# Kernel optimization log

Measured on AMD Instinct MI355X. Metric: run time of the kernel, lower is better.

The kernel has to match this reference:

```python
import jax, jax.numpy as jnp
import numpy as np

B, S, D = 32, 1, 2048
H, KVH, HD = 16, 4, 128
MAXS = 4096
EPS = 1e-5
NREP = H // KVH  # GQA repeat factor = 4
FF = 4 * D
POS = 4095  # decode position (start_pos)


def setup_inputs() -> dict:
    key = jax.random.key(0)
    ks = jax.random.split(key, 12)
    sc = lambda d: 1.0 / np.sqrt(d)
    # RoPE angles for the current token position, [S, HD//2]
    inv_freq = 1.0 / (10000.0 ** (np.arange(0, HD, 2, dtype=np.float32) / HD))
    ang = (POS + np.arange(S, dtype=np.float32))[:, None] * inv_freq[None, :]
    return {
        "x": jax.random.normal(ks[0], (B, S, D), jnp.float32),
        "cos": jnp.asarray(np.cos(ang), jnp.float32),
        "sin": jnp.asarray(np.sin(ang), jnp.float32),
        "k_cache": jax.random.normal(ks[1], (B, MAXS, KVH, HD), jnp.float32),
        "v_cache": jax.random.normal(ks[2], (B, MAXS, KVH, HD), jnp.float32),
        "w_rms_attn": jnp.ones((D,), jnp.float32),
        "wq": jax.random.normal(ks[3], (D, D), jnp.float32) * sc(D),
        "wk": jax.random.normal(ks[4], (D, KVH * HD), jnp.float32) * sc(D),
        "wv": jax.random.normal(ks[5], (D, KVH * HD), jnp.float32) * sc(D),
        "wo": jax.random.normal(ks[6], (D, D), jnp.float32) * sc(D),
        "w_rms_ffn": jnp.ones((D,), jnp.float32),
        "w1": jax.random.normal(ks[7], (D, FF), jnp.float32) * sc(D),
        "w2": jax.random.normal(ks[8], (D, FF), jnp.float32) * sc(D),
        "w3": jax.random.normal(ks[9], (FF, D), jnp.float32) * sc(FF),
        "start_pos": POS,
    }


def _rmsnorm(x, g):
    return x * g * jax.lax.rsqrt(jnp.mean(x * x, axis=-1, keepdims=True) + EPS)


def _rope(x, cos, sin):
    # x: [B, S, h, HD]; complex rotation on (even, odd) pairs
    xr = x.reshape(*x.shape[:-1], HD // 2, 2)
    x0, x1 = xr[..., 0], xr[..., 1]
    c = cos[None, :, None, :]
    s = sin[None, :, None, :]
    r0 = x0 * c - x1 * s
    r1 = x0 * s + x1 * c
    return jnp.stack([r0, r1], axis=-1).reshape(x.shape)


def reference(x, cos, sin, k_cache, v_cache, w_rms_attn, wq, wk, wv, wo,
              w_rms_ffn, w1, w2, w3, start_pos):
    xa = _rmsnorm(x, w_rms_attn)
    xq = (xa @ wq).reshape(B, S, H, HD)
    xk = (xa @ wk).reshape(B, S, KVH, HD)
    xv = (xa @ wv).reshape(B, S, KVH, HD)
    # Source applies RoPE to K and V (not Q) -- reproduced faithfully.
    xk = _rope(xk, cos, sin)
    xv = _rope(xv, cos, sin)
    kc = jax.lax.dynamic_update_slice(k_cache, xk, (0, start_pos, 0, 0))
    vc = jax.lax.dynamic_update_slice(v_cache, xv, (0, start_pos, 0, 0))
    klen = start_pos + S
    keys = jnp.repeat(kc[:, :klen], NREP, axis=2)   # [B, klen, H, HD]
    vals = jnp.repeat(vc[:, :klen], NREP, axis=2)
    att = jnp.einsum('bqhd,bkhd->bhqk', xq, keys) * (HD ** -0.5)
    att = jax.nn.softmax(att, axis=-1)
    y = jnp.einsum('bhqk,bkhd->bqhd', att, vals).reshape(B, S, D)
    h = x + y @ wo
    xf = _rmsnorm(h, w_rms_ffn)
    return h + (jax.nn.silu(xf @ w1) * (xf @ w2)) @ w3
```

## Files before the change

kernel.cpp:

```cpp
#include <hip/hip_runtime.h>
#include <math.h>

#define BB 32
#define DD 2048
#define NKVH 4
#define HDIM 128
#define MAXS 4096
#define FFD 8192
#define POS 4095
#define EPSV 1e-5f
#define SCALE 0.08838834764831845f
#define ASPLIT 32
#define SPOS 128

#define OFF_QT   0u
#define OFF_KT   65536u
#define OFF_VT   81920u
#define OFF_G1   98304u
#define OFF_G2   360448u
#define ZERO_N   622592u
#define OFF_XAT  622592u
#define OFF_PML  720896u
#define OFF_PACC 753664u
#define OFF_YT   2850816u
#define OFF_H    2916352u
#define OFF_XFT  2981888u
#define OFF_KFIX 3047424u
#define OFF_VFIX 3309568u

#define VM_WAIT8  asm volatile("s_waitcnt vmcnt(8)" ::: "memory")
#define VM_WAIT0  asm volatile("s_waitcnt vmcnt(0)" ::: "memory")
#define LG_WAIT0  asm volatile("s_waitcnt lgkmcnt(0)" ::: "memory")
#define SCHED0    __builtin_amdgcn_sched_barrier(0)
#define SBAR      __builtin_amdgcn_s_barrier()

#define REP32(M) M(0) M(1) M(2) M(3) M(4) M(5) M(6) M(7) M(8) M(9) M(10) M(11) M(12) M(13) M(14) M(15) M(16) M(17) M(18) M(19) M(20) M(21) M(22) M(23) M(24) M(25) M(26) M(27) M(28) M(29) M(30) M(31)
#define REP32A(M,X) M(0,X) M(1,X) M(2,X) M(3,X) M(4,X) M(5,X) M(6,X) M(7,X) M(8,X) M(9,X) M(10,X) M(11,X) M(12,X) M(13,X) M(14,X) M(15,X) M(16,X) M(17,X) M(18,X) M(19,X) M(20,X) M(21,X) M(22,X) M(23,X) M(24,X) M(25,X) M(26,X) M(27,X) M(28,X) M(29,X) M(30,X) M(31,X)

#define DECLA(i) float a##i = 0.f;
#define FMA1(i,k) a##i = fmaf(ap[(k)*32 + (i)], w##k, a##i);
#define STORET(i) tl[i] = a##i;
#define ATOMN(i) atomicAdd(C + (size_t)(i)*N + n, a##i);

template<int N, int CH, bool TOUT>
__device__ __forceinline__ void gemv_body(const float* __restrict__ At,
                                          const float* __restrict__ W,
                                          float* __restrict__ C, int colblk,
                                          float* tile) {
    int tid = (int)threadIdx.x;
    int n = colblk * 256 + tid;
    int d0 = blockIdx.y * CH;
    const float* Wp = W + (size_t)d0 * N + n;
    const float* ap = At + (size_t)d0 * 32;
    REP32(DECLA)
#pragma unroll 4
    for (int dd = 0; dd < CH; dd += 4) {
        float w0 = Wp[0];
        float w1 = Wp[(size_t)N];
        float w2 = Wp[(size_t)N * 2];
        float w3 = Wp[(size_t)N * 3];
        REP32A(FMA1, 0)
        REP32A(FMA1, 1)
        REP32A(FMA1, 2)
        REP32A(FMA1, 3)
        Wp += (size_t)N * 4;
        ap += 128;
    }
    if constexpr (TOUT) {
        float* tl = tile + tid * 33;
        REP32(STORET)
        __syncthreads();
        float* cb = C + (size_t)colblk * 256 * 32;
#pragma unroll
        for (int i = 0; i < 32; ++i) {
            int f = i * 256 + tid;
            atomicAdd(cb + f, tile[(f >> 5) * 33 + (f & 31)]);
        }
    } else {
        REP32(ATOMN)
    }
}

template<int N, int CH, bool TOUT>
__global__ __launch_bounds__(256) void gemv32_kernel(const float* __restrict__ At,
                                                     const float* __restrict__ W,
                                                     float* __restrict__ C) {
    if constexpr (TOUT) {
        __shared__ float tile[256 * 33];
        gemv_body<N, CH, true>(At, W, C, blockIdx.x, tile);
    } else {
        gemv_body<N, CH, false>(At, W, C, blockIdx.x, nullptr);
    }
}

template<int N, int CH, int HALF>
__global__ __launch_bounds__(256) void gemv32_dual_kernel(const float* __restrict__ At,
        const float* __restrict__ W0, const float* __restrict__ W1,
        float* __restrict__ C0, float* __restrict__ C1) {
    __shared__ float tile[256 * 33];
    int bx = blockIdx.x;
    if (bx < HALF) gemv_body<N, CH, true>(At, W0, C0, bx, tile);
    else           gemv_body<N, CH, true>(At, W1, C1, bx - HALF, tile);
}

__global__ void zero_rms_kernel(float* __restrict__ p, const float* __restrict__ in,
                                const float* __restrict__ g, float* __restrict__ outT,
                                float* __restrict__ cpy) {
    int bx = blockIdx.x, tid = threadIdx.x;
    if (bx < 608) {
        ((float4*)p)[bx * 256 + tid] = (float4){0.f, 0.f, 0.f, 0.f};
        return;
    }
    int b = bx - 608;
    const float* row = in + b * DD;
    float v[8];
    float ss = 0.f;
#pragma unroll
    for (int i = 0; i < 8; ++i) { v[i] = row[tid + i * 256]; ss += v[i] * v[i]; }
#pragma unroll
    for (int off = 32; off; off >>= 1) ss += __shfl_xor(ss, off);
    __shared__ float red[4];
    if ((tid & 63) == 0) red[tid >> 6] = ss;
    __syncthreads();
    ss = red[0] + red[1] + red[2] + red[3];
    float scale = rsqrtf(ss * (1.f / DD) + EPSV);
#pragma unroll
    for (int i = 0; i < 8; ++i) {
        int idx = tid + i * 256;
        outT[(size_t)idx * 32 + b] = v[i] * g[idx] * scale;
        cpy[b * DD + idx] = v[i];
    }
}

__global__ void rmsnorm_kernel(const float* __restrict__ in, const float* __restrict__ g,
                               float* __restrict__ outT, float* __restrict__ cpy) {
    int b = blockIdx.x;
    int tid = threadIdx.x;
    const float* row = in + b * DD;
    float v[8];
    float ss = 0.f;
#pragma unroll
    for (int i = 0; i < 8; ++i) { v[i] = row[tid + i * 256]; ss += v[i] * v[i]; }
#pragma unroll
    for (int off = 32; off; off >>= 1) ss += __shfl_xor(ss, off);
    __shared__ float red[4];
    if ((tid & 63) == 0) red[tid >> 6] = ss;
    __syncthreads();
    ss = red[0] + red[1] + red[2] + red[3];
    float scale = rsqrtf(ss * (1.f / DD) + EPSV);
#pragma unroll
    for (int i = 0; i < 8; ++i) {
        int idx = tid + i * 256;
        outT[(size_t)idx * 32 + b] = v[i] * g[idx] * scale;
        if (cpy) cpy[b * DD + idx] = v[i];
    }
}

__global__ void fixrope_kernel(const float* __restrict__ kc, const float* __restrict__ vc,
                               const float* __restrict__ kT, const float* __restrict__ vT,
                               const float* __restrict__ cosb, const float* __restrict__ sinb,
                               float* __restrict__ kfix, float* __restrict__ vfix) {
    int idx = blockIdx.x * 256 + threadIdx.x;
    int b = idx >> 12, rem = idx & 4095;
    int pos = rem >> 8, pr = rem & 255;
    int gpos = 4080 + pos;
    float2 kv, vv;
    if (gpos == POS) {
        int hd2 = pr & 63;
        float c = cosb[hd2], s = sinb[hd2];
        int col = pr * 2;
        float k0 = kT[(size_t)col * 32 + b], k1 = kT[(size_t)(col + 1) * 32 + b];
        float v0 = vT[(size_t)col * 32 + b], v1 = vT[(size_t)(col + 1) * 32 + b];
        kv = (float2){k0 * c - k1 * s, k0 * s + k1 * c};
        vv = (float2){v0 * c - v1 * s, v0 * s + v1 * c};
    } else {
        size_t o = ((size_t)(b * MAXS + gpos)) * 256 + pr;
        kv = ((const float2*)kc)[o]; vv = ((const float2*)vc)[o];
    }
    size_t d = (size_t)b * 4096 + pos * 256 + pr;
    ((float2*)kfix)[d] = kv; ((float2*)vfix)[d] = vv;
}

__global__ __launch_bounds__(256, 2) void attn_stage_kernel(
    const float* __restrict__ qn, const float* __restrict__ kc, const float* __restrict__ vc,
    const float* __restrict__ kfix, const float* __restrict__ vfix,
    float* __restrict__ pml, float* __restrict__ pacc) {
    int split = blockIdx.x & 31, b = blockIdx.x >> 5;
    int tid = threadIdx.x, lane = tid & 63, wv = tid >> 6;
    __shared__ float kbuf[2][8192];
    __shared__ float p_s[128][16];
    int qpos = tid >> 4, qhead = tid & 15;
    int qr = qpos * 4 + (qhead >> 2);
    int vh = tid >> 4, c16 = tid & 15, vkvh = vh >> 2;
    int t0 = split * SPOS;

    float4 qrot[32];
#pragma unroll
    for (int j = 0; j < 32; ++j) {
        int g = (j + qr) & 31;
        qrot[j] = *(const float4*)(qn + (size_t)b * DD + qhead * HDIM + g * 4);
    }
    float4 av0 = {0, 0, 0, 0}, av1 = {0, 0, 0, 0};

    auto stage = [&](int t) {
        int s = t & 7;
        const float* base;
        if (t < 8) base = (split == 31 && s == 7) ? kfix + (size_t)b * 8192
                                                  : kc + ((size_t)b * MAXS + t0 + s * 16) * 512;
        else       base = (split == 31 && s == 7) ? vfix + (size_t)b * 8192
                                                  : vc + ((size_t)b * MAXS + t0 + s * 16) * 512;
        const float* g = base + wv * 2048 + lane * 4;
        float* l = &kbuf[t & 1][wv * 2048];
#pragma unroll
        for (int i = 0; i < 8; ++i)
            __builtin_amdgcn_global_load_lds(
                (const __attribute__((address_space(1))) void*)(g + i * 256),
                (__attribute__((address_space(3))) void*)(l + i * 256), 16, 0, 0);
    };

    stage(0);
    for (int t = 0; t < 16; ++t) {
        if (t < 15) { stage(t + 1); VM_WAIT8; } else { VM_WAIT0; }
        SCHED0; SBAR;
        if (t == 8) {
#pragma unroll
            for (int hh = 0; hh < 4; ++hh) {
                int h = wv * 4 + hh;
                float e0 = p_s[lane][h], e1 = p_s[lane + 64][h];
                float m = fmaxf(e0, e1);
#pragma unroll
                for (int off = 32; off; off >>= 1) m = fmaxf(m, __shfl_xor(m, off));
                e0 = __expf(e0 - m); e1 = __expf(e1 - m);
                p_s[lane][h] = e0; p_s[lane + 64][h] = e1;
                float l2 = e0 + e1;
#pragma unroll
                for (int off = 32; off; off >>= 1) l2 += __shfl_xor(l2, off);
                if (lane == 0) {
                    int idx = ((b * ASPLIT + split) * 16 + h) * 2;
                    pml[idx] = m; pml[idx + 1] = l2;
                }
            }
        }
        const float* kb = kbuf[t & 1];
        if (t < 8) {
            float4 acc = {0, 0, 0, 0};
            const float* rowp = kb + qr * 128;
#pragma unroll
            for (int j = 0; j < 32; ++j) {
                int g = (j + qr) & 31;
                float4 k4 = *(const float4*)(rowp + g * 4);
                acc.x = fmaf(k4.x, qrot[j].x, acc.x);
                acc.y = fmaf(k4.y, qrot[j].y, acc.y);
                acc.z = fmaf(k4.z, qrot[j].z, acc.z);
                acc.w = fmaf(k4.w, qrot[j].w, acc.w);
            }
            p_s[t * 16 + qpos][qhead] = (acc.x + acc.y + acc.z + acc.w) * SCALE;
        } else {
            int s = t - 8;
            const float* vrow = kb + vkvh * 128 + c16 * 4;
#pragma unroll
            for (int p = 0; p < 16; ++p) {
                float pw = p_s[s * 16 + p][vh];
                float4 v0 = *(const float4*)(vrow + p * 512);
                float4 v1 = *(const float4*)(vrow + p * 512 + 64);
                av0.x = fmaf(pw, v0.x, av0.x); av0.y = fmaf(pw, v0.y, av0.y);
                av0.z = fmaf(pw, v0.z, av0.z); av0.w = fmaf(pw, v0.w, av0.w);
                av1.x = fmaf(pw, v1.x, av1.x); av1.y = fmaf(pw, v1.y, av1.y);
                av1.z = fmaf(pw, v1.z, av1.z); av1.w = fmaf(pw, v1.w, av1.w);
            }
        }
        LG_WAIT0; SCHED0; SBAR;
    }
    size_t pbase = ((size_t)(b * ASPLIT + split) * 16 + vh) * HDIM;
    *(float4*)(pacc + pbase + c16 * 4) = av0;
    *(float4*)(pacc + pbase + 64 + c16 * 4) = av1;
}

__global__ void attn_combine_kernel(const float* __restrict__ pml,
                                    const float* __restrict__ pacc, float* __restrict__ yT) {
    int bid = blockIdx.x;
    int b = bid >> 4, h = bid & 15;
    int d = threadIdx.x;
    float M = -INFINITY;
#pragma unroll 8
    for (int s = 0; s < ASPLIT; ++s)
        M = fmaxf(M, pml[((b * ASPLIT + s) * 16 + h) * 2]);
    float denom = 0.f, acc = 0.f;
#pragma unroll 4
    for (int s = 0; s < ASPLIT; ++s) {
        int idx = (b * ASPLIT + s) * 16 + h;
        float e = __expf(pml[idx * 2] - M);
        denom += pml[idx * 2 + 1] * e;
        acc += e * pacc[(size_t)idx * HDIM + d];
    }
    yT[(size_t)(h * HDIM + d) * 32 + b] = acc / denom;
}

__global__ void silu_mul_kernel(float* __restrict__ g1, const float* __restrict__ g2) {
    int i = blockIdx.x * 256 + threadIdx.x;
    float4 a = ((const float4*)g1)[i];
    float4 b4 = ((const float4*)g2)[i];
    a.x = a.x * b4.x / (1.f + __expf(-a.x));
    a.y = a.y * b4.y / (1.f + __expf(-a.y));
    a.z = a.z * b4.z / (1.f + __expf(-a.z));
    a.w = a.w * b4.w / (1.f + __expf(-a.w));
    ((float4*)g1)[i] = a;
}

extern "C" void kernel_launch(void* const* d_in, const int* in_sizes, int n_in,
                              void* d_out, int out_size, void* d_ws, size_t ws_size,
                              hipStream_t stream) {
    (void)in_sizes; (void)n_in; (void)out_size; (void)ws_size;
    const float* x    = (const float*)d_in[0];
    const float* cosb = (const float*)d_in[1];
    const float* sinb = (const float*)d_in[2];
    const float* kc   = (const float*)d_in[3];
    const float* vc   = (const float*)d_in[4];
    const float* wra  = (const float*)d_in[5];
    const float* wq   = (const float*)d_in[6];
    const float* wk   = (const float*)d_in[7];
    const float* wv   = (const float*)d_in[8];
    const float* wo   = (const float*)d_in[9];
    const float* wrf  = (const float*)d_in[10];
    const float* w1   = (const float*)d_in[11];
    const float* w2   = (const float*)d_in[12];
    const float* w3   = (const float*)d_in[13];
    float* out = (float*)d_out;
    float* ws  = (float*)d_ws;

    float* qn   = ws + OFF_QT;
    float* kT   = ws + OFF_KT;
    float* vT   = ws + OFF_VT;
    float* g1T  = ws + OFF_G1;
    float* g2T  = ws + OFF_G2;
    float* xaT  = ws + OFF_XAT;
    float* pml  = ws + OFF_PML;
    float* pacc = ws + OFF_PACC;
    float* yT   = ws + OFF_YT;
    float* h    = ws + OFF_H;
    float* xfT  = ws + OFF_XFT;
    float* kfix = ws + OFF_KFIX;
    float* vfix = ws + OFF_VFIX;

    zero_rms_kernel<<<640, 256, 0, stream>>>(ws, x, wra, xaT, h);
    gemv32_kernel<2048, 64, false><<<dim3(8, 32), 256, 0, stream>>>(xaT, wq, qn);
    gemv32_dual_kernel<512, 32, 2><<<dim3(4, 64), 256, 0, stream>>>(xaT, wk, wv, kT, vT);
    fixrope_kernel<<<512, 256, 0, stream>>>(kc, vc, kT, vT, cosb, sinb, kfix, vfix);
    attn_stage_kernel<<<1024, 256, 0, stream>>>(qn, kc, vc, kfix, vfix, pml, pacc);
    attn_combine_kernel<<<512, 128, 0, stream>>>(pml, pacc, yT);
    gemv32_kernel<2048, 64, false><<<dim3(8, 32), 256, 0, stream>>>(yT, wo, h);
    rmsnorm_kernel<<<32, 256, 0, stream>>>(h, wrf, xfT, out);
    gemv32_dual_kernel<8192, 256, 32><<<dim3(64, 8), 256, 0, stream>>>(xfT, w1, w2, g1T, g2T);
    silu_mul_kernel<<<256, 256, 0, stream>>>(g1T, g2T);
    gemv32_kernel<2048, 128, false><<<dim3(8, 64), 256, 0, stream>>>(g1T, w3, out);
}
```

Baseline: 305.2 us.

## Fuse QKV GEMVs, fold RoPE fix into attention, retune GEMV chunks

Replaces the separate Q and dual K/V GEMV launches with a single QKV GEMV kernel that writes non-transposed outputs. It drops the fixrope kernel and its kfix/vfix copies, and the attention kernel now computes RoPE for the new token directly into LDS for the last tile while skipping that row's global load. It also halves the GEMV chunk sizes for the wo and w1/w2 GEMVs so more blocks are launched. The goal is fewer launches and less extra traffic, at the cost of a divergent branch in the attention kernel plus some risk around LDS write ordering and the hardcoded N in the dual kernel.

Result: faster. 292.2 us (-4.3%).

```diff
diff --git a/kernel.cpp b/kernel.cpp
--- a/kernel.cpp
+++ b/kernel.cpp
@@ -13,9 +13,9 @@
 #define ASPLIT 32
 #define SPOS 128
 
-#define OFF_QT   0u
-#define OFF_KT   65536u
-#define OFF_VT   81920u
+#define OFF_QN   0u
+#define OFF_KN   65536u
+#define OFF_VN   81920u
 #define OFF_G1   98304u
 #define OFF_G2   360448u
 #define ZERO_N   622592u
@@ -25,8 +25,6 @@
 #define OFF_YT   2850816u
 #define OFF_H    2916352u
 #define OFF_XFT  2981888u
-#define OFF_KFIX 3047424u
-#define OFF_VFIX 3309568u
 
 #define VM_WAIT8  asm volatile("s_waitcnt vmcnt(8)" ::: "memory")
 #define VM_WAIT0  asm volatile("s_waitcnt vmcnt(0)" ::: "memory")
@@ -99,8 +97,18 @@
         float* __restrict__ C0, float* __restrict__ C1) {
     __shared__ float tile[256 * 33];
     int bx = blockIdx.x;
-    if (bx < HALF) gemv_body<N, CH, true>(At, W0, C0, bx, tile);
-    else           gemv_body<N, CH, true>(At, W1, C1, bx - HALF, tile);
+    if (bx < HALF) gemv_body<8192, CH, true>(At, W0, C0, bx, tile);
+    else           gemv_body<8192, CH, true>(At, W1, C1, bx - HALF, tile);
+}
+
+__global__ __launch_bounds__(256) void gemv_qkv_kernel(const float* __restrict__ At,
+        const float* __restrict__ wq, const float* __restrict__ wk,
+        const float* __restrict__ wv, float* __restrict__ qn,
+        float* __restrict__ kn, float* __restrict__ vn) {
+    int bx = blockIdx.x;
+    if (bx < 8)       gemv_body<2048, 32, false>(At, wq, qn, bx, nullptr);
+    else if (bx < 10) gemv_body<512, 32, false>(At, wk, kn, bx - 8, nullptr);
+    else              gemv_body<512, 32, false>(At, wv, vn, bx - 10, nullptr);
 }
 
 __global__ void zero_rms_kernel(float* __restrict__ p, const float* __restrict__ in,
@@ -156,34 +164,10 @@
     }
 }
 
-__global__ void fixrope_kernel(const float* __restrict__ kc, const float* __restrict__ vc,
-                               const float* __restrict__ kT, const float* __restrict__ vT,
-                               const float* __restrict__ cosb, const float* __restrict__ sinb,
-                               float* __restrict__ kfix, float* __restrict__ vfix) {
-    int idx = blockIdx.x * 256 + threadIdx.x;
-    int b = idx >> 12, rem = idx & 4095;
-    int pos = rem >> 8, pr = rem & 255;
-    int gpos = 4080 + pos;
-    float2 kv, vv;
-    if (gpos == POS) {
-        int hd2 = pr & 63;
-        float c = cosb[hd2], s = sinb[hd2];
-        int col = pr * 2;
-        float k0 = kT[(size_t)col * 32 + b], k1 = kT[(size_t)(col + 1) * 32 + b];
-        float v0 = vT[(size_t)col * 32 + b], v1 = vT[(size_t)(col + 1) * 32 + b];
-        kv = (float2){k0 * c - k1 * s, k0 * s + k1 * c};
-        vv = (float2){v0 * c - v1 * s, v0 * s + v1 * c};
-    } else {
-        size_t o = ((size_t)(b * MAXS + gpos)) * 256 + pr;
-        kv = ((const float2*)kc)[o]; vv = ((const float2*)vc)[o];
-    }
-    size_t d = (size_t)b * 4096 + pos * 256 + pr;
-    ((float2*)kfix)[d] = kv; ((float2*)vfix)[d] = vv;
-}
-
 __global__ __launch_bounds__(256, 2) void attn_stage_kernel(
     const float* __restrict__ qn, const float* __restrict__ kc, const float* __restrict__ vc,
-    const float* __restrict__ kfix, const float* __restrict__ vfix,
+    const float* __restrict__ kn, const float* __restrict__ vn,
+    const float* __restrict__ cosb, const float* __restrict__ sinb,
     float* __restrict__ pml, float* __restrict__ pacc) {
     int split = blockIdx.x & 31, b = blockIdx.x >> 5;
     int tid = threadIdx.x, lane = tid & 63, wv = tid >> 6;
@@ -204,23 +188,39 @@
 
     auto stage = [&](int t) {
         int s = t & 7;
-        const float* base;
-        if (t < 8) base = (split == 31 && s == 7) ? kfix + (size_t)b * 8192
-                                                  : kc + ((size_t)b * MAXS + t0 + s * 16) * 512;
-        else       base = (split == 31 && s == 7) ? vfix + (size_t)b * 8192
-                                                  : vc + ((size_t)b * MAXS + t0 + s * 16) * 512;
+        const float* base = (t < 8) ? kc + ((size_t)b * MAXS + t0 + s * 16) * 512
+                                    : vc + ((size_t)b * MAXS + t0 + s * 16) * 512;
         const float* g = base + wv * 2048 + lane * 4;
         float* l = &kbuf[t & 1][wv * 2048];
+        int imax = (split == 31 && s == 7 && wv == 3) ? 6 : 8;
 #pragma unroll
         for (int i = 0; i < 8; ++i)
-            __builtin_amdgcn_global_load_lds(
-                (const __attribute__((address_space(1))) void*)(g + i * 256),
-                (__attribute__((address_space(3))) void*)(l + i * 256), 16, 0, 0);
+            if (i < imax)
+                __builtin_amdgcn_global_load_lds(
+                    (const __attribute__((address_space(1))) void*)(g + i * 256),
+                    (__attribute__((address_space(3))) void*)(l + i * 256), 16, 0, 0);
     };
 
     stage(0);
     for (int t = 0; t < 16; ++t) {
-        if (t < 15) { stage(t + 1); VM_WAIT8; } else { VM_WAIT0; }
+        if (t < 15) {
+            stage(t + 1);
+            if (split == 31 && wv == 3 && (t == 6 || t == 14)) {
+                const float* src = (t == 6) ? kn : vn;
+                float* dst = &kbuf[(t + 1) & 1][7680 + lane * 8];
+                int col0 = lane * 8;
+#pragma unroll
+                for (int m = 0; m < 4; ++m) {
+                    int col = col0 + 2 * m;
+                    int ci = (col & 127) >> 1;
+                    float cc = cosb[ci], ssn = sinb[ci];
+                    float x0 = src[b * 512 + col], x1 = src[b * 512 + col + 1];
+                    dst[2 * m]     = x0 * cc - x1 * ssn;
+                    dst[2 * m + 1] = x0 * ssn + x1 * cc;
+                }
+            }
+            VM_WAIT8;
+        } else { VM_WAIT0; }
         SCHED0; SBAR;
         if (t == 8) {
 #pragma unroll
@@ -328,9 +328,9 @@
     float* out = (float*)d_out;
     float* ws  = (float*)d_ws;
 
-    float* qn   = ws + OFF_QT;
-    float* kT   = ws + OFF_KT;
-    float* vT   = ws + OFF_VT;
+    float* qn   = ws + OFF_QN;
+    float* kn   = ws + OFF_KN;
+    float* vn   = ws + OFF_VN;
     float* g1T  = ws + OFF_G1;
     float* g2T  = ws + OFF_G2;
     float* xaT  = ws + OFF_XAT;
@@ -339,18 +339,14 @@
     float* yT   = ws + OFF_YT;
     float* h    = ws + OFF_H;
     float* xfT  = ws + OFF_XFT;
-    float* kfix = ws + OFF_KFIX;
-    float* vfix = ws + OFF_VFIX;
 
     zero_rms_kernel<<<640, 256, 0, stream>>>(ws, x, wra, xaT, h);
-    gemv32_kernel<2048, 64, false><<<dim3(8, 32), 256, 0, stream>>>(xaT, wq, qn);
-    gemv32_dual_kernel<512, 32, 2><<<dim3(4, 64), 256, 0, stream>>>(xaT, wk, wv, kT, vT);
-    fixrope_kernel<<<512, 256, 0, stream>>>(kc, vc, kT, vT, cosb, sinb, kfix, vfix);
-    attn_stage_kernel<<<1024, 256, 0, stream>>>(qn, kc, vc, kfix, vfix, pml, pacc);
+    gemv_qkv_kernel<<<dim3(12, 64), 256, 0, stream>>>(xaT, wq, wk, wv, qn, kn, vn);
+    attn_stage_kernel<<<1024, 256, 0, stream>>>(qn, kc, vc, kn, vn, cosb, sinb, pml, pacc);
     attn_combine_kernel<<<512, 128, 0, stream>>>(pml, pacc, yT);
-    gemv32_kernel<2048, 64, false><<<dim3(8, 32), 256, 0, stream>>>(yT, wo, h);
+    gemv32_kernel<2048, 32, false><<<dim3(8, 64), 256, 0, stream>>>(yT, wo, h);
     rmsnorm_kernel<<<32, 256, 0, stream>>>(h, wrf, xfT, out);
-    gemv32_dual_kernel<8192, 256, 32><<<dim3(64, 8), 256, 0, stream>>>(xfT, w1, w2, g1T, g2T);
+    gemv32_dual_kernel<8192, 128, 32><<<dim3(64, 16), 256, 0, stream>>>(xfT, w1, w2, g1T, g2T);
     silu_mul_kernel<<<256, 256, 0, stream>>>(g1T, g2T);
     gemv32_kernel<2048, 128, false><<<dim3(8, 64), 256, 0, stream>>>(g1T, w3, out);
 }
```
